# Kernel tuning notes

Measured on AMD Instinct MI355X. Metric: run time of the kernel, lower is better.

Reference implementation:

```python
import jax, jax.numpy as jnp
import numpy as np

LEFT = [4, 5, 6, 11, 12, 13]
RIGHT = [1, 2, 3, 14, 15, 16]
MID = [0, 7, 8, 9, 10]
NUM_HEADS = 4
NUM_LAYERS = 4
LN_EPS = 1e-5


def _cols(idx):
    return [i * 2 for i in idx] + [i * 2 + 1 for i in idx]


def setup_inputs() -> dict:
    key = jax.random.key(0)
    D, B, n, N, L, BR = 512, 128, 250, 251, NUM_LAYERS, 3
    ks = jax.random.split(key, 24)

    def rn(k, shape, scale):
        return jax.random.normal(k, shape, dtype=jnp.float32) * jnp.float32(scale)

    s = 1.0 / np.sqrt(D)  # xavier-like scale for DxD weights
    return {
        "x": rn(ks[0], (B, n, 34), 1.0),
        "w_left": rn(ks[1], (12, D), 1.0 / np.sqrt(12)),
        "b_left": jnp.full((D,), 0.1, jnp.float32),
        "w_right": rn(ks[2], (12, D), 1.0 / np.sqrt(12)),
        "b_right": jnp.full((D,), 0.1, jnp.float32),
        "w_mid": rn(ks[3], (10, D), 1.0 / np.sqrt(10)),
        "b_mid": jnp.full((D,), 0.1, jnp.float32),
        "pos_emb": rn(ks[4], (1, N, D), 1.0),
        "cls_token": rn(ks[5], (1, 1, D), 1.0),
        "ln1_g": jnp.ones((BR, L, D), jnp.float32),
        "ln1_b": jnp.zeros((BR, L, D), jnp.float32),
        "ln2_g": jnp.ones((BR, L, D), jnp.float32),
        "ln2_b": jnp.zeros((BR, L, D), jnp.float32),
        "wq": rn(ks[6], (BR, L, D, D), s),
        "wk": rn(ks[7], (BR, L, D, D), s),
        "wv": rn(ks[8], (BR, L, D, D), s),
        "wo": rn(ks[9], (BR, L, D, D), s),
        "fc1_w": rn(ks[10], (BR, L, D, D), s),
        "fc1_b": jnp.full((BR, L, D), 0.1, jnp.float32),
        "fc2_w": rn(ks[11], (BR, L, D, D), s),
        "fc2_b": jnp.full((BR, L, D), 0.1, jnp.float32),
        "out1_w": rn(ks[12], (3 * D, D), 1.0 / np.sqrt(3 * D)),
        "out1_b": jnp.full((D,), 0.1, jnp.float32),
        "out2_w": rn(ks[13], (D, 1), s),
        "out2_b": jnp.full((1,), 0.1, jnp.float32),
    }


def _layernorm(z, g, b):
    mu = jnp.mean(z, axis=-1, keepdims=True)
    var = jnp.var(z, axis=-1, keepdims=True)
    return (z - mu) * jax.lax.rsqrt(var + LN_EPS) * g + b


def _attention(z, Wq, Wk, Wv, Wo):
    b, n, d = z.shape
    hd = d // NUM_HEADS
    def heads(w):
        return (z @ w).reshape(b, n, NUM_HEADS, hd).transpose(0, 2, 1, 3)
    q, k, v = heads(Wq), heads(Wk), heads(Wv)
    logits = jnp.einsum("bhqd,bhkd->bhqk", q, k) / jnp.sqrt(jnp.float32(hd))
    attn = jax.nn.softmax(logits, axis=-1)
    o = jnp.einsum("bhqk,bhkd->bhqd", attn, v).transpose(0, 2, 1, 3).reshape(b, n, d)
    return o @ Wo


def reference(x, w_left, b_left, w_right, b_right, w_mid, b_mid, pos_emb, cls_token,
              ln1_g, ln1_b, ln2_g, ln2_b, wq, wk, wv, wo,
              fc1_w, fc1_b, fc2_w, fc2_b, out1_w, out1_b, out2_w, out2_b):
    b, n, _ = x.shape
    embeds = [
        x[:, :, _cols(LEFT)] @ w_left + b_left,
        x[:, :, _cols(RIGHT)] @ w_right + b_right,
        x[:, :, _cols(MID)] @ w_mid + b_mid,
    ]
    cls = jnp.broadcast_to(cls_token, (b, 1, cls_token.shape[-1]))
    cls_outs = []
    for br in range(3):
        h = jnp.concatenate([cls, embeds[br]], axis=1) + pos_emb[:, : n + 1, :]
        for l in range(NUM_LAYERS):
            h = h + _attention(_layernorm(h, ln1_g[br, l], ln1_b[br, l]),
                               wq[br, l], wk[br, l], wv[br, l], wo[br, l])
            m = _layernorm(h, ln2_g[br, l], ln2_b[br, l])
            m = jax.nn.gelu(m @ fc1_w[br, l] + fc1_b[br, l], approximate=False)
            h = h + (m @ fc2_w[br, l] + fc2_b[br, l])
        cls_outs.append(h[:, 0, :])
    cat = jnp.concatenate(cls_outs, axis=-1)  # [b, 3*D]
    hid = jax.nn.gelu(cat @ out1_w + out1_b, approximate=False)
    out = hid @ out2_w + out2_b  # [b, 1]
    return jax.nn.sigmoid(out).squeeze()
```

## Files before the change

kernel.cpp:

```cpp
#include <hip/hip_runtime.h>
#include <math.h>

#define DD   512
#define BATCH 128
#define NTOK 251
#define NHEAD 4
#define HD   128

#define GF_ADDC   1
#define GF_BIAS   2
#define GF_GELU   4
#define GF_OBF16  8
#define GF_LN     16

typedef unsigned short ushort_t;
typedef __attribute__((ext_vector_type(8))) short bf16x8;
typedef __attribute__((ext_vector_type(4))) float f32x4;

__constant__ int c_cols[3][12] = {
  {8,10,12,22,24,26, 9,11,13,23,25,27},
  {2, 4, 6,28,30,32, 3, 5, 7,29,31,33},
  {0,14,16,18,20, 1,15,17,19,21, 0, 0}
};
__constant__ int c_ncols[3] = {12,12,10};

__device__ __forceinline__ float gelu_f(float v){
  return 0.5f*v*(1.0f + erff(v*0.70710678118654752440f));
}
__device__ __forceinline__ ushort_t f2b(float v){
  union { float f; unsigned u; } x; x.f = v;
  unsigned r = x.u + 0x7fffu + ((x.u >> 16) & 1u);
  return (ushort_t)(r >> 16);
}
__device__ __forceinline__ float b2f(ushort_t u){
  union { unsigned u; float f; } x; x.u = ((unsigned)u) << 16; return x.f;
}
__device__ __forceinline__ void async_copy16(const void* g, void* l){
  __builtin_amdgcn_global_load_lds(
      (const __attribute__((address_space(1))) unsigned*)g,
      (__attribute__((address_space(3))) unsigned*)l, 16, 0, 0);
}

__global__ __launch_bounds__(256) void wtrans_kernel(ushort_t* __restrict__ dst,
                                                     const float* __restrict__ src,
                                                     long ldD, long dstPlane, long srcPlane){
  __shared__ float tile[32][33];
  long mat = blockIdx.z;
  const float* S = src + mat*srcPlane;
  ushort_t* D = dst + mat*dstPlane;
  int n0 = blockIdx.x*32, k0 = blockIdx.y*32;
  for (int r = threadIdx.y; r < 32; r += 8)
    tile[r][threadIdx.x] = S[(long)(k0+r)*DD + n0 + threadIdx.x];
  __syncthreads();
  for (int r = threadIdx.y; r < 32; r += 8)
    D[(long)(n0+r)*ldD + k0 + threadIdx.x] = f2b(tile[threadIdx.x][r]);
}

__global__ __launch_bounds__(256) void wpack_kernel(ushort_t* __restrict__ dst,
                                                    const float* __restrict__ src,
                                                    long dstPlane, long srcPlane){
  int c = blockIdx.x;
  int nb = c >> 4, kc = c & 15;
  long mat = blockIdx.z;
  const float* S = src + mat*srcPlane;
  ushort_t* D = dst + mat*dstPlane + (long)c*2048;
  int t = threadIdx.x;
  int j = t >> 6, lane = t & 63;
  int quad = lane >> 4, l15 = lane & 15;
  int n = nb*64 + j*16 + l15;
  int k = kc*32 + quad*8;
  ushort_t o8[8];
  #pragma unroll
  for (int e = 0; e < 8; e++) o8[e] = f2b(S[(long)(k+e)*512 + n]);
  *(uint4*)(D + (j*64 + lane)*8) = *(const uint4*)o8;
}

__global__ void embed_kernel(ushort_t* __restrict__ h, const float* __restrict__ x,
                             const float* __restrict__ w, const float* __restrict__ bias,
                             const float* __restrict__ pos, const float* __restrict__ cls,
                             int br, int b0){
  long bt = blockIdx.x;
  int  t  = (int)(bt % NTOK);
  long b  = b0 + bt / NTOK;
  ushort_t* outr = h + bt*DD;
  if (t == 0){
    for (int d = threadIdx.x; d < DD; d += 128) outr[d] = f2b(cls[d] + pos[d]);
    return;
  }
  const float* xr = x + (b*(NTOK-1) + (t-1))*34;
  int nc = c_ncols[br];
  float xs[12];
  for (int j = 0; j < 12; j++) xs[j] = (j < nc) ? xr[c_cols[br][j]] : 0.0f;
  const float* posr = pos + (long)t*DD;
  for (int d = threadIdx.x; d < DD; d += 128){
    float acc = bias[d] + posr[d];
    for (int j = 0; j < nc; j++) acc = fmaf(xs[j], w[j*DD + d], acc);
    outr[d] = f2b(acc);
  }
}

__global__ __launch_bounds__(256) void vtrans_kernel(ushort_t* __restrict__ vt,
                                                     const ushort_t* __restrict__ v){
  __shared__ ushort_t tile[32][33];
  int b = blockIdx.z >> 2, hh = blockIdx.z & 3;
  const ushort_t* src = v + (long)b*NTOK*1536 + hh*HD;
  ushort_t* dst = vt + (long)blockIdx.z*HD*256;
  int t0 = blockIdx.y*32, d0 = blockIdx.x*32;
  int tx = threadIdx.x, ty = threadIdx.y;
  for (int r = ty; r < 32; r += 8){
    int t = t0 + r;
    tile[r][tx] = (t < NTOK) ? src[(long)t*1536 + d0 + tx] : (ushort_t)0;
  }
  __syncthreads();
  for (int r = ty; r < 32; r += 8)
    dst[(long)(d0 + r)*256 + t0 + tx] = tile[tx][r];
}

__global__ __launch_bounds__(512, 2) void flash_kernel(
    ushort_t* __restrict__ o, const ushort_t* __restrict__ qkv,
    const ushort_t* __restrict__ vt, float alpha){
  __shared__ __align__(16) ushort_t Ks[256*16*8];
  __shared__ __align__(16) ushort_t Vs[128*32*8];
  __shared__ __align__(16) ushort_t Ps[8][32*40];
  int bh = blockIdx.x, b = bh>>2, hh = bh&3;
  const ushort_t* Qg = qkv + (long)b*NTOK*1536 + hh*HD;
  const ushort_t* Kg = Qg + 512;
  const ushort_t* Vg = vt + (long)bh*HD*256;
  int tid = threadIdx.x, w = tid>>6, lane = tid&63;
  int quad = lane>>4, l15 = lane&15;
  int swz = l15 & 7;

  bf16x8 qf[2][4];
  #pragma unroll
  for (int qs = 0; qs < 2; qs++){
    int qrow = w*32 + qs*16 + l15;
    bool qv = qrow < NTOK;
    const ushort_t* qptr = Qg + (long)qrow*1536;
    #pragma unroll
    for (int kc = 0; kc < 4; kc++)
      qf[qs][kc] = qv ? *(const bf16x8*)(qptr + kc*32 + quad*8)
                      : (bf16x8){0,0,0,0,0,0,0,0};
  }

  #pragma unroll
  for (int i = 0; i < 8; i++){
    int base = (w*8 + i)*64;
    int unit = base + lane;
    int t = unit >> 4, u = unit & 15;
    const ushort_t* src = Kg + (long)(t < NTOK ? t : 0)*1536 + ((u ^ (t&7)) << 3);
    async_copy16(src, (void*)&Ks[base*8]);
  }
  #pragma unroll
  for (int i = 0; i < 8; i++){
    int base = (w*8 + i)*64;
    int unit = base + lane;
    int d = unit >> 5, u = unit & 31;
    const ushort_t* src = Vg + (long)d*256 + ((u ^ (d&7)) << 3);
    async_copy16(src, (void*)&Vs[base*8]);
  }
  __syncthreads();

  f32x4 oacc[2][8] = {};
  float mrow[2][4], lrow[2][4];
  #pragma unroll
  for (int qs = 0; qs < 2; qs++)
    #pragma unroll
    for (int r = 0; r < 4; r++){ mrow[qs][r] = -1e30f; lrow[qs][r] = 0.0f; }

  ushort_t* Psw = &Ps[w][0];

  for (int c = 0; c < 8; c++){
    f32x4 s[2][2] = {};
    #pragma unroll
    for (int kc = 0; kc < 4; kc++){
      #pragma unroll
      for (int j = 0; j < 2; j++){
        int t = c*32 + j*16 + l15;
        bf16x8 bf = *(const bf16x8*)&Ks[(t*16 + ((kc*4 + quad) ^ swz))*8];
        s[0][j] = __builtin_amdgcn_mfma_f32_16x16x32_bf16(qf[0][kc], bf, s[0][j], 0, 0, 0);
        s[1][j] = __builtin_amdgcn_mfma_f32_16x16x32_bf16(qf[1][kc], bf, s[1][j], 0, 0, 0);
      }
    }
    #pragma unroll
    for (int qs = 0; qs < 2; qs++){
      #pragma unroll
      for (int r = 0; r < 4; r++){
        int t0 = c*32 + l15, t1 = t0 + 16;
        float v0 = (t0 < NTOK) ? s[qs][0][r]*alpha : -1e30f;
        float v1 = (t1 < NTOK) ? s[qs][1][r]*alpha : -1e30f;
        float mx = fmaxf(v0, v1);
        mx = fmaxf(mx, __shfl_xor(mx,1)); mx = fmaxf(mx, __shfl_xor(mx,2));
        mx = fmaxf(mx, __shfl_xor(mx,4)); mx = fmaxf(mx, __shfl_xor(mx,8));
        float Mn  = fmaxf(mrow[qs][r], mx);
        float fac = __expf(mrow[qs][r] - Mn);
        mrow[qs][r] = Mn;
        float e0 = __expf(v0 - Mn), e1 = __expf(v1 - Mn);
        float sum = e0 + e1;
        sum += __shfl_xor(sum,1); sum += __shfl_xor(sum,2);
        sum += __shfl_xor(sum,4); sum += __shfl_xor(sum,8);
        lrow[qs][r] = lrow[qs][r]*fac + sum;
        #pragma unroll
        for (int j = 0; j < 8; j++) oacc[qs][j][r] *= fac;
        Psw[(qs*16 + quad*4 + r)*40 + l15]      = f2b(e0);
        Psw[(qs*16 + quad*4 + r)*40 + 16 + l15] = f2b(e1);
      }
    }
    bf16x8 af0 = *(const bf16x8*)&Psw[(long)l15*40 + quad*8];
    bf16x8 af1 = *(const bf16x8*)&Psw[(long)(16 + l15)*40 + quad*8];
    #pragma unroll
    for (int j = 0; j < 8; j++){
      int d = j*16 + l15;
      bf16x8 bfv = *(const bf16x8*)&Vs[(d*32 + ((c*4 + quad) ^ swz))*8];
      oacc[0][j] = __builtin_amdgcn_mfma_f32_16x16x32_bf16(af0, bfv, oacc[0][j], 0, 0, 0);
      oacc[1][j] = __builtin_amdgcn_mfma_f32_16x16x32_bf16(af1, bfv, oacc[1][j], 0, 0, 0);
    }
  }

  #pragma unroll
  for (int qs = 0; qs < 2; qs++){
    #pragma unroll
    for (int r = 0; r < 4; r++){
      int q = w*32 + qs*16 + quad*4 + r;
      if (q >= NTOK) continue;
      float invl = 1.0f / lrow[qs][r];
      ushort_t* orow = o + ((long)b*NTOK + q)*512 + hh*128;
      #pragma unroll
      for (int j = 0; j < 8; j++)
        orow[j*16 + l15] = f2b(oacc[qs][j][r]*invl);
    }
  }
}

__global__ __launch_bounds__(512, 2) void lngemm_kernel(
    const ushort_t* __restrict__ A,
    const ushort_t* __restrict__ Bt,
    void* __restrict__ Cp, long ldc,
    const float* __restrict__ lng, const float* __restrict__ lnbeta,
    const float* __restrict__ bias,
    int M, int N, int flags, float alpha){
  __shared__ __align__(16) ushort_t As[128*512];
  int tid = threadIdx.x, w = tid>>6, lane = tid&63;
  int quad = lane>>4, l15 = lane&15;
  int m0 = blockIdx.x*128;

  #pragma unroll
  for (int i = 0; i < 16; i++){
    int row = i*8 + w;
    int gr = m0 + row; if (gr >= M) gr = M - 1;
    const ushort_t* src = A + (long)gr*512 + ((lane ^ (row&7)) << 3);
    async_copy16(src, (void*)&As[row*512]);
  }
  __syncthreads();

  if (flags & GF_LN){
    const float* gp = lng + lane*8;
    const float* bp = lnbeta + lane*8;
    float4 g0 = *(const float4*)gp, g1 = *(const float4*)(gp+4);
    float4 e0 = *(const float4*)bp, e1 = *(const float4*)(bp+4);
    float gg[8] = {g0.x,g0.y,g0.z,g0.w,g1.x,g1.y,g1.z,g1.w};
    float bb[8] = {e0.x,e0.y,e0.z,e0.w,e1.x,e1.y,e1.z,e1.w};
    for (int j = 0; j < 16; j++){
      int r = w*16 + j;
      ushort_t* prow = &As[r*512 + ((lane ^ (r&7)) << 3)];
      union { uint4 v; ushort_t s[8]; } raw;
      raw.v = *(const uint4*)prow;
      float d[8];
      #pragma unroll
      for (int e = 0; e < 8; e++) d[e] = b2f(raw.s[e]);
      float s = 0.0f;
      #pragma unroll
      for (int e = 0; e < 8; e++) s += d[e];
      #pragma unroll
      for (int o = 32; o > 0; o >>= 1) s += __shfl_xor(s, o, 64);
      float mu = s * (1.0f/512.0f);
      float q = 0.0f;
      #pragma unroll
      for (int e = 0; e < 8; e++){ d[e] -= mu; q += d[e]*d[e]; }
      #pragma unroll
      for (int o = 32; o > 0; o >>= 1) q += __shfl_xor(q, o, 64);
      float rr = rsqrtf(q*(1.0f/512.0f) + 1e-5f);
      ushort_t o8[8];
      #pragma unroll
      for (int e = 0; e < 8; e++) o8[e] = f2b(d[e]*rr*gg[e] + bb[e]);
      *(uint4*)prow = *(const uint4*)o8;
    }
  }
  __syncthreads();

  int wm = (w>>2)*64, nbw = (w&3);
  int NT = N >> 8;
  const ushort_t* Bw = Bt + (long)nbw*32768 + lane*8;

  bf16x8 buf[4][4];
  #pragma unroll
  for (int s = 0; s < 4; s++)
    #pragma unroll
    for (int j = 0; j < 4; j++)
      buf[s][j] = *(const bf16x8*)(Bw + s*2048 + j*512);

  for (int nt = 0; nt < NT; nt++){
    long nxt = (nt + 1 < NT) ? 4L*32768 : 0;
    f32x4 acc[4][4] = {};
    #pragma unroll
    for (int kc = 0; kc < 16; kc++){
      bf16x8 af[4];
      #pragma unroll
      for (int i = 0; i < 4; i++){
        int row = wm + i*16 + l15;
        af[i] = *(const bf16x8*)&As[row*512 + (((kc*4+quad) ^ (row&7)) << 3)];
      }
      #pragma unroll
      for (int i = 0; i < 4; i++)
        #pragma unroll
        for (int j = 0; j < 4; j++)
          acc[i][j] = __builtin_amdgcn_mfma_f32_16x16x32_bf16(af[i], buf[kc&3][j], acc[i][j], 0, 0, 0);
      if (kc < 12){
        #pragma unroll
        for (int j = 0; j < 4; j++)
          buf[kc&3][j] = *(const bf16x8*)(Bw + (kc+4)*2048 + j*512);
      } else {
        #pragma unroll
        for (int j = 0; j < 4; j++)
          buf[kc&3][j] = *(const bf16x8*)(Bw + nxt + (kc-12)*2048 + j*512);
      }
    }
    #pragma unroll
    for (int i = 0; i < 4; i++){
      int rbase = m0 + wm + i*16 + quad*4;
      #pragma unroll
      for (int j = 0; j < 4; j++){
        int gn = nt*256 + nbw*64 + j*16 + l15;
        #pragma unroll
        for (int r = 0; r < 4; r++){
          int gm = rbase + r;
          if (gm >= M) continue;
          float v = acc[i][j][r] * alpha;
          if (flags & GF_BIAS) v += bias[gn];
          if (flags & GF_ADDC) v += b2f(((const ushort_t*)Cp)[(long)gm*ldc + gn]);
          if (flags & GF_GELU) v = gelu_f(v);
          if (flags & GF_OBF16) ((ushort_t*)Cp)[(long)gm*ldc + gn] = f2b(v);
          else                  ((float*)Cp)[(long)gm*ldc + gn] = v;
        }
      }
    }
    Bw += 4L*32768;
  }
}

__global__ __launch_bounds__(256) void gemm_bt_mfma(
    const ushort_t* __restrict__ A, long lda, long sA1, long sA2,
    const ushort_t* __restrict__ Bt, long ldb, long sB1, long sB2,
    void* __restrict__ Cp, long ldc, long sC1, long sC2,
    const float* __restrict__ bias, int M, int N, int K,
    int zdiv, int flags, float alpha){
  int bz = blockIdx.z;
  A  += (long)(bz/zdiv)*sA1 + (long)(bz%zdiv)*sA2;
  Bt += (long)(bz/zdiv)*sB1 + (long)(bz%zdiv)*sB2;
  long coff = (long)(bz/zdiv)*sC1 + (long)(bz%zdiv)*sC2;

  __shared__ __align__(16) ushort_t As[128*32];
  __shared__ __align__(16) ushort_t Bs[128*32];

  int tid = threadIdx.x;
  int wave = tid >> 6, lane = tid & 63;
  int quad = lane >> 4, l15 = lane & 15;
  int wm = (wave >> 1) * 64, wn = (wave & 1) * 64;
  int m0 = blockIdx.y * 128, n0 = blockIdx.x * 128;

  f32x4 acc[4][4] = {};
  bool fast = (m0 + 128 <= M) && (n0 + 128 <= N) && ((K & 31) == 0);

  if (fast){
    int rloc = wave*16 + (lane >> 2);
    int pos  = lane & 3;
    const ushort_t* A0 = A + (long)m0*lda;
    const ushort_t* B0 = Bt + (long)n0*ldb;
    for (int k0 = 0; k0 < K; k0 += 32){
      #pragma unroll
      for (int c = 0; c < 2; c++){
        int r  = c*64 + rloc;
        int cg = pos ^ ((r >> 1) & 3);
        long koff = k0 + cg*8;
        async_copy16(A0 + (long)r*lda + koff, (void*)&As[(c*256 + wave*64)*8]);
        async_copy16(B0 + (long)r*ldb + koff, (void*)&Bs[(c*256 + wave*64)*8]);
      }
      __syncthreads();
      bf16x8 af[4], bfv[4];
      #pragma unroll
      for (int i = 0; i < 4; i++){
        int row = wm + i*16 + l15;
        af[i] = *(const bf16x8*)&As[row*32 + ((quad ^ ((row>>1)&3)) << 3)];
      }
      #pragma unroll
      for (int j = 0; j < 4; j++){
        int row = wn + j*16 + l15;
        bfv[j] = *(const bf16x8*)&Bs[row*32 + ((quad ^ ((row>>1)&3)) << 3)];
      }
      #pragma unroll
      for (int i = 0; i < 4; i++)
        #pragma unroll
        for (int j = 0; j < 4; j++)
          acc[i][j] = __builtin_amdgcn_mfma_f32_16x16x32_bf16(af[i], bfv[j], acc[i][j], 0, 0, 0);
      __syncthreads();
    }
  } else {
    int nk = (K + 31) >> 5;
    for (int kt = 0; kt < nk; kt++){
      int k0 = kt << 5;
      #pragma unroll
      for (int c = 0; c < 2; c++){
        int q = c*256 + tid;
        int r = q >> 2;
        int gk = k0 + (((q & 3) ^ ((r >> 1) & 3)) << 3);
        {
          int gm = m0 + r;
          uint4 va;
          if (gm < M && gk + 8 <= K){
            va = *(const uint4*)(A + (long)gm*lda + gk);
          } else {
            ushort_t t[8];
            #pragma unroll
            for (int e = 0; e < 8; e++){
              int kk = gk + e;
              t[e] = (gm < M && kk < K) ? A[(long)gm*lda + kk] : (ushort_t)0;
            }
            va = *(const uint4*)t;
          }
          *(uint4*)&As[r*32 + (q & 3)*8] = va;
        }
        {
          int gn = n0 + r;
          uint4 vb;
          if (gn < N && gk + 8 <= K){
            vb = *(const uint4*)(Bt + (long)gn*ldb + gk);
          } else {
            ushort_t t[8];
            #pragma unroll
            for (int e = 0; e < 8; e++){
              int kk = gk + e;
              t[e] = (gn < N && kk < K) ? Bt[(long)gn*ldb + kk] : (ushort_t)0;
            }
            vb = *(const uint4*)t;
          }
          *(uint4*)&Bs[r*32 + (q & 3)*8] = vb;
        }
      }
      __syncthreads();
      bf16x8 af[4], bfv[4];
      #pragma unroll
      for (int i = 0; i < 4; i++){
        int row = wm + i*16 + l15;
        af[i] = *(const bf16x8*)&As[row*32 + ((quad ^ ((row>>1)&3)) << 3)];
      }
      #pragma unroll
      for (int j = 0; j < 4; j++){
        int row = wn + j*16 + l15;
        bfv[j] = *(const bf16x8*)&Bs[row*32 + ((quad ^ ((row>>1)&3)) << 3)];
      }
      #pragma unroll
      for (int i = 0; i < 4; i++)
        #pragma unroll
        for (int j = 0; j < 4; j++)
          acc[i][j] = __builtin_amdgcn_mfma_f32_16x16x32_bf16(af[i], bfv[j], acc[i][j], 0, 0, 0);
      __syncthreads();
    }
  }

  #pragma unroll
  for (int i = 0; i < 4; i++){
    int rbase = m0 + wm + i*16 + quad*4;
    #pragma unroll
    for (int j = 0; j < 4; j++){
      int gn = n0 + wn + j*16 + l15;
      if (gn >= N) continue;
      #pragma unroll
      for (int r = 0; r < 4; r++){
        int gm = rbase + r;
        if (gm >= M) continue;
        float v = acc[i][j][r] * alpha;
        if (flags & GF_BIAS) v += bias[gn];
        if (flags & GF_ADDC){
          if (flags & GF_OBF16) v += b2f(((const ushort_t*)Cp)[coff + (long)gm*ldc + gn]);
          else                  v += ((const float*)Cp)[coff + (long)gm*ldc + gn];
        }
        if (flags & GF_GELU) v = gelu_f(v);
        if (flags & GF_OBF16){
          ((ushort_t*)Cp)[coff + (long)gm*ldc + gn] = f2b(v);
        } else {
          ((float*)Cp)[coff + (long)gm*ldc + gn] = v;
        }
      }
    }
  }
}

__global__ void copy_cls(ushort_t* __restrict__ cat, const ushort_t* __restrict__ h,
                         int br, int b0){
  long b = blockIdx.x;
  int d = threadIdx.x;
  cat[(b0+b)*1536 + (long)br*512 + d] = h[b*(long)NTOK*DD + d];
}

__global__ void head2_kernel(float* __restrict__ out, const float* __restrict__ hid,
                             const float* __restrict__ w2, const float* __restrict__ b2){
  __shared__ float sbuf[8];
  long b = blockIdx.x;
  float v = hid[b*DD + threadIdx.x] * w2[threadIdx.x];
  #pragma unroll
  for (int o = 32; o > 0; o >>= 1) v += __shfl_down(v, o, 64);
  if ((threadIdx.x & 63) == 0) sbuf[threadIdx.x>>6] = v;
  __syncthreads();
  if (threadIdx.x == 0){
    float s = 0.0f;
    #pragma unroll
    for (int i = 0; i < 8; i++) s += sbuf[i];
    out[b] = 1.0f/(1.0f + expf(-(s + b2[0])));
  }
}

static size_t ws_needed(int Bc){
  auto al = [](size_t b){ return ((b + 255)/256)*256; };
  size_t BNc = (size_t)Bc*NTOK;
  size_t tot = 0;
  tot += al((12UL*1536 + 36UL*512 + 512UL)*512*2 + 512UL*1024*2);
  tot += al(BNc*DD*2);
  tot += al(BNc*DD*2);
  tot += al(BNc*1536*2);
  tot += al((size_t)Bc*NHEAD*HD*256*2);
  tot += al(128UL*1536*2) + al(128UL*512*4);
  tot += 4096;
  return tot;
}

extern "C" void kernel_launch(void* const* d_in, const int* in_sizes, int n_in,
                              void* d_out, int out_size, void* d_ws, size_t ws_size,
                              hipStream_t stream){
  (void)in_sizes; (void)n_in; (void)out_size;
  const float* x      = (const float*)d_in[0];
  const float* w_left = (const float*)d_in[1];
  const float* b_left = (const float*)d_in[2];
  const float* w_right= (const float*)d_in[3];
  const float* b_right= (const float*)d_in[4];
  const float* w_mid  = (const float*)d_in[5];
  const float* b_mid  = (const float*)d_in[6];
  const float* pos    = (const float*)d_in[7];
  const float* cls    = (const float*)d_in[8];
  const float* ln1_g  = (const float*)d_in[9];
  const float* ln1_b  = (const float*)d_in[10];
  const float* ln2_g  = (const float*)d_in[11];
  const float* ln2_b  = (const float*)d_in[12];
  const float* wq     = (const float*)d_in[13];
  const float* wk     = (const float*)d_in[14];
  const float* wv     = (const float*)d_in[15];
  const float* wo     = (const float*)d_in[16];
  const float* fc1w   = (const float*)d_in[17];
  const float* fc1b   = (const float*)d_in[18];
  const float* fc2w   = (const float*)d_in[19];
  const float* fc2b   = (const float*)d_in[20];
  const float* o1w    = (const float*)d_in[21];
  const float* o1b    = (const float*)d_in[22];
  const float* o2w    = (const float*)d_in[23];
  const float* o2b    = (const float*)d_in[24];
  float* out = (float*)d_out;

  int Bc = 128;
  while (Bc > 1 && ws_needed(Bc) > ws_size) Bc >>= 1;
  const int nchunk = BATCH / Bc;
  const long BNc  = (long)Bc*NTOK;

  char* wsp = (char*)d_ws;
  auto carveb = [&](size_t bytes)->void*{
    void* p = (void*)wsp;
    wsp += ((bytes + 255)/256)*256;
    return p;
  };
  ushort_t* wt   = (ushort_t*)carveb((12UL*1536 + 36UL*512 + 512UL)*512*2 + 512UL*1024*2);
  ushort_t* h    = (ushort_t*)carveb(BNc*DD*2);
  ushort_t* z    = (ushort_t*)carveb(BNc*DD*2);
  ushort_t* qkv  = (ushort_t*)carveb(BNc*1536*2);
  ushort_t* vt   = (ushort_t*)carveb((size_t)Bc*NHEAD*HD*256*2);
  ushort_t* cat  = (ushort_t*)carveb(128UL*1536*2);
  float*    hid  = (float*)   carveb(128UL*512*4);

  ushort_t* wtqkv = wt;
  ushort_t* wto   = wt + 12UL*1536*512;
  ushort_t* wt1   = wto + 12UL*512*512;
  ushort_t* wt2   = wt1 + 12UL*512*512;
  ushort_t* wth   = wt2 + 12UL*512*512;

  {
    dim3 gp(128, 1, 12), bp(256);
    long dpq = 1536L*512, dps = 512L*512;
    wpack_kernel<<<gp,bp,0,stream>>>(wtqkv,              wq,   dpq, dps);
    wpack_kernel<<<gp,bp,0,stream>>>(wtqkv + 8L*32768,   wk,   dpq, dps);
    wpack_kernel<<<gp,bp,0,stream>>>(wtqkv + 16L*32768,  wv,   dpq, dps);
    wpack_kernel<<<gp,bp,0,stream>>>(wto,                wo,   dps, dps);
    wpack_kernel<<<gp,bp,0,stream>>>(wt1,                fc1w, dps, dps);
    wpack_kernel<<<gp,bp,0,stream>>>(wt2,                fc2w, dps, dps);
    wtrans_kernel<<<dim3(16,48,1),dim3(32,8),0,stream>>>(wth, o1w, 1536, 0, 0);
  }

  const float* wsel[3] = {w_left, w_right, w_mid};
  const float* bsel[3] = {b_left, b_right, b_mid};

  const float alpha = 0.08838834764831845f;
  int mt = (int)((BNc + 127)/128);
  dim3 gpanel(mt, 1, 1);
  dim3 gvt(4, 8, Bc*NHEAD);

  for (int br = 0; br < 3; br++){
    for (int c = 0; c < nchunk; c++){
      int b0 = c*Bc;
      embed_kernel<<<(int)BNc, 128, 0, stream>>>(h, x, wsel[br], bsel[br], pos, cls, br, b0);
      for (int l = 0; l < 4; l++){
        long wi = (long)br*4 + l;
        const float* g1 = ln1_g + wi*DD; const float* be1 = ln1_b + wi*DD;
        const float* g2 = ln2_g + wi*DD; const float* be2 = ln2_b + wi*DD;
        const ushort_t* Wqkv = wtqkv + wi*1536*512;
        const ushort_t* Wo   = wto + wi*DD*DD;
        const ushort_t* F1   = wt1 + wi*DD*DD;
        const ushort_t* F2   = wt2 + wi*DD*DD;
        const float* F1b = fc1b + wi*DD;  const float* F2b = fc2b + wi*DD;

        lngemm_kernel<<<gpanel, 512, 0, stream>>>(h, Wqkv, qkv, 1536, g1, be1,
                                                  nullptr, (int)BNc, 1536,
                                                  GF_LN|GF_OBF16, 1.0f);
        vtrans_kernel<<<gvt, dim3(32,8), 0, stream>>>(vt, qkv + 1024);
        flash_kernel<<<dim3(Bc*NHEAD), dim3(512), 0, stream>>>(z, qkv, vt, alpha);
        lngemm_kernel<<<gpanel, 512, 0, stream>>>(z, Wo, h, 512, nullptr, nullptr,
                                                  nullptr, (int)BNc, 512,
                                                  GF_ADDC|GF_OBF16, 1.0f);
        lngemm_kernel<<<gpanel, 512, 0, stream>>>(h, F1, qkv, 512, g2, be2,
                                                  F1b, (int)BNc, 512,
                                                  GF_LN|GF_BIAS|GF_GELU|GF_OBF16, 1.0f);
        lngemm_kernel<<<gpanel, 512, 0, stream>>>(qkv, F2, h, 512, nullptr, nullptr,
                                                  F2b, (int)BNc, 512,
                                                  GF_BIAS|GF_ADDC|GF_OBF16, 1.0f);
      }
      copy_cls<<<Bc, 512, 0, stream>>>(cat, h, br, b0);
    }
  }
  dim3 ghd(4, 1, 1);
  gemm_bt_mfma<<<ghd, dim3(256), 0, stream>>>(cat,1536,0,0, wth,1536,0,0, hid,DD,0,0, o1b,
                                              128,DD,1536, 1, GF_BIAS|GF_GELU, 1.0f);
  head2_kernel<<<BATCH, 512, 0, stream>>>(out, hid, o2w, o2b);
}
```

Measured before the change: 4.742 ms.

## Stage LN-GEMM B tiles through double-buffered LDS with async copies

Replaces the per-wave register prefetch of B fragments from global memory in the LN-fused GEMM with cooperative async copies into a double-buffered LDS tile, so each B chunk is fetched once per block instead of once per wave pair. This removes duplicated global loads of B across the two M-halves of waves. In exchange it adds a __syncthreads per k-chunk, more LDS use (32KB extra on top of 128KB As), and shorter prefetch distance (one chunk ahead instead of four), which may hurt occupancy and latency hiding.

New measurement: 5.123 ms. 8.0% more time.

```diff
diff --git a/kernel.cpp b/kernel.cpp
--- a/kernel.cpp
+++ b/kernel.cpp
@@ -239,9 +239,15 @@
     const float* __restrict__ bias,
     int M, int N, int flags, float alpha){
   __shared__ __align__(16) ushort_t As[128*512];
+  __shared__ __align__(16) ushort_t Bs[2][8192];
   int tid = threadIdx.x, w = tid>>6, lane = tid&63;
   int quad = lane>>4, l15 = lane&15;
   int m0 = blockIdx.x*128;
+
+  int nb0 = w >> 2,        jj0 = w & 3;
+  int nb1 = (8 + w) >> 2,  jj1 = (8 + w) & 3;
+  long boff0 = (long)jj0*512 + lane*8;
+  long boff1 = (long)jj1*512 + lane*8;
 
   #pragma unroll
   for (int i = 0; i < 16; i++){
@@ -249,6 +255,12 @@
     int gr = m0 + row; if (gr >= M) gr = M - 1;
     const ushort_t* src = A + (long)gr*512 + ((lane ^ (row&7)) << 3);
     async_copy16(src, (void*)&As[row*512]);
+  }
+  {
+    const ushort_t* s0 = Bt + (long)nb0*16*2048 + boff0;
+    const ushort_t* s1 = Bt + (long)nb1*16*2048 + boff1;
+    async_copy16(s0, (void*)&Bs[0][nb0*2048 + jj0*512]);
+    async_copy16(s1, (void*)&Bs[0][nb1*2048 + jj1*512]);
   }
   __syncthreads();
 
@@ -287,42 +299,37 @@
   }
   __syncthreads();
 
-  int wm = (w>>2)*64, nbw = (w&3);
+  int wm = (w>>2)*64, nbw = w & 3;
   int NT = N >> 8;
-  const ushort_t* Bw = Bt + (long)nbw*32768 + lane*8;
-
-  bf16x8 buf[4][4];
-  #pragma unroll
-  for (int s = 0; s < 4; s++)
-    #pragma unroll
-    for (int j = 0; j < 4; j++)
-      buf[s][j] = *(const bf16x8*)(Bw + s*2048 + j*512);
-
   for (int nt = 0; nt < NT; nt++){
-    long nxt = (nt + 1 < NT) ? 4L*32768 : 0;
     f32x4 acc[4][4] = {};
     #pragma unroll
     for (int kc = 0; kc < 16; kc++){
-      bf16x8 af[4];
+      int ntp, kcp;
+      if (kc < 15){ ntp = nt; kcp = kc + 1; }
+      else { bool more = (nt + 1 < NT); ntp = more ? nt + 1 : nt; kcp = more ? 0 : 15; }
+      {
+        const ushort_t* s0 = Bt + ((long)(ntp*4 + nb0)*16 + kcp)*2048 + boff0;
+        const ushort_t* s1 = Bt + ((long)(ntp*4 + nb1)*16 + kcp)*2048 + boff1;
+        async_copy16(s0, (void*)&Bs[(kc+1)&1][nb0*2048 + jj0*512]);
+        async_copy16(s1, (void*)&Bs[(kc+1)&1][nb1*2048 + jj1*512]);
+      }
+      const ushort_t* Bp = &Bs[kc&1][nbw*2048];
+      bf16x8 af[4], bv[4];
       #pragma unroll
       for (int i = 0; i < 4; i++){
         int row = wm + i*16 + l15;
         af[i] = *(const bf16x8*)&As[row*512 + (((kc*4+quad) ^ (row&7)) << 3)];
       }
       #pragma unroll
+      for (int j = 0; j < 4; j++)
+        bv[j] = *(const bf16x8*)(Bp + (long)j*512 + lane*8);
+      #pragma unroll
       for (int i = 0; i < 4; i++)
         #pragma unroll
         for (int j = 0; j < 4; j++)
-          acc[i][j] = __builtin_amdgcn_mfma_f32_16x16x32_bf16(af[i], buf[kc&3][j], acc[i][j], 0, 0, 0);
-      if (kc < 12){
-        #pragma unroll
-        for (int j = 0; j < 4; j++)
-          buf[kc&3][j] = *(const bf16x8*)(Bw + (kc+4)*2048 + j*512);
-      } else {
-        #pragma unroll
-        for (int j = 0; j < 4; j++)
-          buf[kc&3][j] = *(const bf16x8*)(Bw + nxt + (kc-12)*2048 + j*512);
-      }
+          acc[i][j] = __builtin_amdgcn_mfma_f32_16x16x32_bf16(af[i], bv[j], acc[i][j], 0, 0, 0);
+      __syncthreads();
     }
     #pragma unroll
     for (int i = 0; i < 4; i++){
@@ -343,7 +350,6 @@
         }
       }
     }
-    Bw += 4L*32768;
   }
 }
 
```
